# Kernel tuning notes

Hardware: AMD Instinct MI355X
Metric: run time of the kernel (lower is better)

Reference implementation:

```python
import jax, jax.numpy as jnp
import numpy as np

EMBED_DIM = 768
NUM_HEADS = 12
HEAD_DIM = EMBED_DIM // NUM_HEADS
SCALE = HEAD_DIM ** -0.5
LN_EPS = 1e-5


def layer_norm(x, gamma, beta):
    mu = jnp.mean(x, axis=-1, keepdims=True)
    var = jnp.var(x, axis=-1, keepdims=True)
    return (x - mu) * jax.lax.rsqrt(var + LN_EPS) * gamma + beta


def setup_inputs() -> dict:
    key = jax.random.key(0)
    ks = jax.random.split(key, 10)
    B, N, M, C = 4, 4096, 256, EMBED_DIM
    inp = {
        "input_tokens": jax.random.normal(ks[0], (B, N, C), dtype=jnp.float32),
        "query_tokens": jax.random.normal(ks[1], (B, M, C), dtype=jnp.float32),
        "Wq": jax.random.normal(ks[2], (C, C), dtype=jnp.float32) * 0.02,
        "bq": jnp.zeros((C,), dtype=jnp.float32),
        "Wk": jax.random.normal(ks[3], (C, C), dtype=jnp.float32) * 0.02,
        "bk": jnp.zeros((C,), dtype=jnp.float32),
        "Wv": jax.random.normal(ks[4], (C, C), dtype=jnp.float32) * 0.02,
        "bv": jnp.zeros((C,), dtype=jnp.float32),
        "gq_ln": jnp.ones((C,), dtype=jnp.float32),
        "bq_ln": jnp.zeros((C,), dtype=jnp.float32),
        "gk_ln": jnp.ones((C,), dtype=jnp.float32),
        "bk_ln": jnp.zeros((C,), dtype=jnp.float32),
    }
    return inp


def reference(input_tokens, query_tokens, Wq, bq, Wk, bk, Wv, bv,
              gq_ln, bq_ln, gk_ln, bk_ln):
    B, N, C = input_tokens.shape
    _, M, _ = query_tokens.shape
    H, D = NUM_HEADS, HEAD_DIM

    # v: Linear only (no LayerNorm on the attn=None path)
    v = (input_tokens @ Wv.T + bv).reshape(B, N, H, D).transpose(0, 2, 1, 3)   # [B,H,N,D]
    # q, k: Linear -> LayerNorm over full embed_dim, then split heads
    q = layer_norm(query_tokens @ Wq.T + bq, gq_ln, bq_ln)
    q = q.reshape(B, M, H, D).transpose(0, 2, 1, 3) * SCALE                    # [B,H,M,D]
    k = layer_norm(input_tokens @ Wk.T + bk, gk_ln, bk_ln)
    k = k.reshape(B, N, H, D).transpose(0, 2, 1, 3)                            # [B,H,N,D]

    attn = jax.nn.softmax(jnp.einsum('bhmd,bhnd->bhmn', q, k), axis=-1)        # [B,H,M,N]
    out = jnp.einsum('bhmn,bhnd->bhmd', attn, v)                               # [B,H,M,D]
    out = out.transpose(0, 2, 1, 3).reshape(B, M, C)
    return (query_tokens + out, attn)
```

## Files before the change

### kernel.cpp

```cpp
#include <hip/hip_runtime.h>
#include <math.h>

#define BB 4
#define NN 4096
#define MM 256
#define CC 768
#define HH 12
#define DD 64
#define SCALEF 0.125f
#define LN_EPSF 1e-5f

typedef __attribute__((ext_vector_type(4))) float f32x4;
typedef __attribute__((ext_vector_type(16))) float f32x16;
typedef __attribute__((ext_vector_type(8))) _Float16 f16x8;
typedef __attribute__((ext_vector_type(4))) _Float16 f16x4;

__device__ __forceinline__ void gldh(const _Float16* g, _Float16* l) {
    __builtin_amdgcn_global_load_lds(
        (const __attribute__((address_space(1))) void*)g,
        (__attribute__((address_space(3))) void*)l, 16, 0, 0);
}

__global__ __launch_bounds__(256) void conv_all(
    const float* __restrict__ x0, _Float16* __restrict__ y0, long long n0,
    const float* __restrict__ x1, _Float16* __restrict__ y1, long long n1,
    const float* __restrict__ x2, _Float16* __restrict__ y2, long long n2,
    const float* __restrict__ x3, _Float16* __restrict__ y3, long long n3,
    const float* __restrict__ x4, _Float16* __restrict__ y4, long long n4)
{
    long long i = ((long long)blockIdx.x * 256 + threadIdx.x) * 8;
    const long long total = n0 + n1 + n2 + n3 + n4;
    const long long stride = (long long)gridDim.x * 256 * 8;
    for (; i < total; i += stride) {
        const float* x; _Float16* y; long long off = i;
        if (off < n0) { x = x0; y = y0; }
        else if ((off -= n0) < n1) { x = x1; y = y1; }
        else if ((off -= n1) < n2) { x = x2; y = y2; }
        else if ((off -= n2) < n3) { x = x3; y = y3; }
        else { off -= n3; x = x4; y = y4; }
        float4 a = *(const float4*)(x + off);
        float4 b = *(const float4*)(x + off + 4);
        f16x8 o;
        o[0] = (_Float16)a.x; o[1] = (_Float16)a.y;
        o[2] = (_Float16)a.z; o[3] = (_Float16)a.w;
        o[4] = (_Float16)b.x; o[5] = (_Float16)b.y;
        o[6] = (_Float16)b.z; o[7] = (_Float16)b.w;
        *(f16x8*)(y + off) = o;
    }
}

__global__ __launch_bounds__(256) void proj_kv_f16(
    const _Float16* __restrict__ Xh,
    const _Float16* __restrict__ X2h,
    const _Float16* __restrict__ Wkh, const _Float16* __restrict__ Wqh,
    const _Float16* __restrict__ Wvh,
    const float* __restrict__ bk, const float* __restrict__ bq,
    const float* __restrict__ bv,
    _Float16* __restrict__ Klin, _Float16* __restrict__ Qlin,
    _Float16* __restrict__ Vth)
{
    __shared__ _Float16 As[2][4096];
    __shared__ _Float16 Bks[2][4096];
    __shared__ _Float16 Bvs[2][4096];

    const int bid = blockIdx.x;
    const _Float16* Ag; const _Float16* Bkg;
    const float* biask; _Float16* outk;
    bool hasV;
    int bm, bn;
    if (bid < 768) {
        bm = bid & 127; bn = bid >> 7;
        Ag = Xh; Bkg = Wkh; biask = bk; outk = Klin; hasV = true;
    } else {
        const int sid = bid - 768;
        bm = sid & 7; bn = sid >> 3;
        Ag = X2h; Bkg = Wqh; biask = bq; outk = Qlin; hasV = false;
    }
    const int row0 = bm * 128, col0 = bn * 128;

    const int tid = threadIdx.x;
    const int w = tid >> 6, lane = tid & 63;
    const int wr = w >> 1, wc = w & 1;
    const int fr = lane & 15, kg = lane >> 4;

    f32x4 acck[4][4], accv[4][4];
#pragma unroll
    for (int m = 0; m < 4; ++m)
#pragma unroll
        for (int n = 0; n < 4; ++n) {
            acck[m][n] = (f32x4){0.f, 0.f, 0.f, 0.f};
            accv[m][n] = (f32x4){0.f, 0.f, 0.f, 0.f};
        }

#define STAGE(sel, kt)                                                           \
    do {                                                                         \
        const int kk = (kt) << 5;                                                \
        _Pragma("unroll")                                                        \
        for (int i = 0; i < 2; ++i) {                                            \
            const int cbase = (i * 4 + w) * 64;                                  \
            const int c = cbase + lane;                                          \
            const int row = c >> 2, ks = (c & 3) << 3;                           \
            gldh(Ag  + (size_t)(row0 + row) * CC + kk + ks, &As[sel][cbase * 8]);\
            gldh(Bkg + (size_t)(col0 + row) * CC + kk + ks, &Bks[sel][cbase * 8]);\
            gldh(Wvh + (size_t)(col0 + row) * CC + kk + ks, &Bvs[sel][cbase * 8]);\
        }                                                                        \
    } while (0)

    STAGE(0, 0);
    int cur = 0;
    const int nk = CC >> 5;
    for (int kt = 0; kt < nk; ++kt) {
        __syncthreads();
        if (kt + 1 < nk) STAGE(cur ^ 1, kt + 1);
        const _Float16* lA = As[cur];
        const _Float16* lBk = Bks[cur];
        const _Float16* lBv = Bvs[cur];
        f16x8 a[4];
#pragma unroll
        for (int m = 0; m < 4; ++m)
            a[m] = *(const f16x8*)(lA + (wr * 64 + m * 16 + fr) * 32 + kg * 8);
#pragma unroll
        for (int n = 0; n < 4; ++n) {
            f16x8 bkf = *(const f16x8*)(lBk + (wc * 64 + n * 16 + fr) * 32 + kg * 8);
            __builtin_amdgcn_s_setprio(1);
#pragma unroll
            for (int m = 0; m < 4; ++m)
                acck[m][n] = __builtin_amdgcn_mfma_f32_16x16x32_f16(
                    a[m], bkf, acck[m][n], 0, 0, 0);
            __builtin_amdgcn_s_setprio(0);
            f16x8 bvf = *(const f16x8*)(lBv + (wc * 64 + n * 16 + fr) * 32 + kg * 8);
            __builtin_amdgcn_s_setprio(1);
#pragma unroll
            for (int m = 0; m < 4; ++m)
                accv[m][n] = __builtin_amdgcn_mfma_f32_16x16x32_f16(
                    a[m], bvf, accv[m][n], 0, 0, 0);
            __builtin_amdgcn_s_setprio(0);
        }
        cur ^= 1;
    }
#undef STAGE

    {
        float bvv[4];
#pragma unroll
        for (int n = 0; n < 4; ++n)
            bvv[n] = biask[col0 + wc * 64 + n * 16 + fr];
#pragma unroll
        for (int m = 0; m < 4; ++m)
#pragma unroll
            for (int n = 0; n < 4; ++n) {
                const int col = col0 + wc * 64 + n * 16 + fr;
#pragma unroll
                for (int r = 0; r < 4; ++r) {
                    const int row = row0 + wr * 64 + m * 16 + kg * 4 + r;
                    outk[(size_t)row * CC + col] = (_Float16)(acck[m][n][r] + bvv[n]);
                }
            }
    }
    if (hasV) {
        const int b = row0 >> 12;
        const int rb = row0 & 4095;
#pragma unroll
        for (int n = 0; n < 4; ++n) {
            const int cg = col0 + wc * 64 + n * 16 + fr;
            const int hh = cg >> 6, d = cg & 63;
            const float bb = bv[cg];
            _Float16* vrow = Vth + ((size_t)((b * HH + hh) * DD + d)) * NN + rb + wr * 64;
#pragma unroll
            for (int m = 0; m < 4; ++m) {
                f16x4 v4;
#pragma unroll
                for (int r = 0; r < 4; ++r)
                    v4[r] = (_Float16)(accv[m][n][r] + bb);
                *(f16x4*)(vrow + m * 16 + kg * 4) = v4;
            }
        }
    }
}

__global__ __launch_bounds__(256) void ln_rows_f16(
    const _Float16* __restrict__ Y, _Float16* __restrict__ outh,
    const float* __restrict__ g, const float* __restrict__ be, const float scale)
{
    const int row = blockIdx.x;
    const _Float16* y = Y + (size_t)row * CC;
    const int tid = threadIdx.x;
    float x0 = (float)y[tid], x1 = (float)y[tid + 256], x2 = (float)y[tid + 512];
    float s = x0 + x1 + x2;
    float q = x0 * x0 + x1 * x1 + x2 * x2;
#pragma unroll
    for (int o = 32; o >= 1; o >>= 1) {
        s += __shfl_xor(s, o, 64);
        q += __shfl_xor(q, o, 64);
    }
    __shared__ float sh_s[4], sh_q[4];
    const int w = tid >> 6;
    if ((tid & 63) == 0) { sh_s[w] = s; sh_q[w] = q; }
    __syncthreads();
    s = sh_s[0] + sh_s[1] + sh_s[2] + sh_s[3];
    q = sh_q[0] + sh_q[1] + sh_q[2] + sh_q[3];
    const float mu  = s * (1.f / 768.f);
    const float var = q * (1.f / 768.f) - mu * mu;
    const float inv = rsqrtf(var + LN_EPSF);
    _Float16* o = outh + (size_t)row * CC;
    o[tid]       = (_Float16)(((x0 - mu) * inv * g[tid]       + be[tid])       * scale);
    o[tid + 256] = (_Float16)(((x1 - mu) * inv * g[tid + 256] + be[tid + 256]) * scale);
    o[tid + 512] = (_Float16)(((x2 - mu) * inv * g[tid + 512] + be[tid + 512]) * scale);
}

__global__ __launch_bounds__(256, 4) void attn_stats(
    const _Float16* __restrict__ Qh,
    const _Float16* __restrict__ Kh,
    float* __restrict__ stats)
{
    __shared__ __align__(16) unsigned char smem[37888];
    _Float16* Kl = (_Float16*)smem;
    _Float16* Ql = (_Float16*)(smem + 32768);
    float (*red)[32][2] = (float(*)[32][2])(smem + 36864);

    const int tid = threadIdx.x;
    const int w = tid >> 6, lane = tid & 63;
    const int l5 = lane >> 5, lm = lane & 31;
    const int bid = blockIdx.x;
    const int mt = bid / 192;
    const int rem = bid % 192;
    const int bh = rem >> 2, ns = rem & 3;
    const int h = bh % HH, b = bh / HH;
    const int qr0 = mt * 32;
    const int nb = ns * 1024;

#define STAGEK(sel, c0)                                                         \
    _Pragma("unroll")                                                           \
    for (int i = 0; i < 4; ++i) {                                               \
        const int L = i * 256 + tid;                                            \
        const int n = L >> 3, pos = L & 7;                                      \
        gldh(Kh + (size_t)(b * NN + (c0) + n) * CC + h * DD + ((pos ^ (n & 7)) << 3), \
             &Kl[(sel) * 8192 + (i * 256 + w * 64) * 8]);                       \
    }

    {
        const int n = tid >> 3, pos = tid & 7;
        gldh(Qh + (size_t)(b * MM + qr0 + n) * CC + h * DD + ((pos ^ (n & 7)) << 3),
             &Ql[(w * 64) * 8]);
    }
    STAGEK(0, nb);
    __syncthreads();
    f16x8 qf[4];
#pragma unroll
    for (int ks = 0; ks < 4; ++ks)
        qf[ks] = *(const f16x8*)&Ql[lm * 64 + (((ks * 2 + l5) ^ (lm & 7)) << 3)];

    const int nl = w * 32 + lm;

    float mrun = -1e30f, srun = 0.f;
    int cur = 0;
    for (int c = 0; c < 8; ++c) {
        if (c) __syncthreads();
        if (c + 1 < 8) STAGEK(cur ^ 1, nb + (c + 1) * 128);
        const _Float16* Kb = Kl + cur * 8192;
        f32x16 s;
#pragma unroll
        for (int r = 0; r < 16; ++r) s[r] = 0.f;
        __builtin_amdgcn_s_setprio(1);
#pragma unroll
        for (int ks = 0; ks < 4; ++ks) {
            f16x8 kf = *(const f16x8*)&Kb[nl * 64 + (((ks * 2 + l5) ^ (nl & 7)) << 3)];
            s = __builtin_amdgcn_mfma_f32_32x32x16_f16(kf, qf[ks], s, 0, 0, 0);
        }
        __builtin_amdgcn_s_setprio(0);
        float cmax = s[0];
#pragma unroll
        for (int r = 1; r < 16; ++r) cmax = fmaxf(cmax, s[r]);
        cmax = fmaxf(cmax, __shfl_xor(cmax, 32, 64));
        const float nm = fmaxf(mrun, cmax);
        float cs = 0.f;
#pragma unroll
        for (int r = 0; r < 16; ++r) cs += __expf(s[r] - nm);
        cs += __shfl_xor(cs, 32, 64);
        srun = srun * __expf(mrun - nm) + cs;
        mrun = nm;
        cur ^= 1;
    }
    if (lane < 32) { red[w][lane][0] = mrun; red[w][lane][1] = srun; }
    __syncthreads();
    if (w == 0 && lane < 32) {
        float M = -1e30f;
#pragma unroll
        for (int ww = 0; ww < 4; ++ww) M = fmaxf(M, red[ww][lane][0]);
        float S = 0.f;
#pragma unroll
        for (int ww = 0; ww < 4; ++ww) S += red[ww][lane][1] * __expf(red[ww][lane][0] - M);
        float* sp = stats + ((size_t)((bh * 8 + mt) * 32 + lane)) * 8 + ns * 2;
        sp[0] = M; sp[1] = S;
    }
#undef STAGEK
}

__global__ __launch_bounds__(256, 2) void attn_main(
    const _Float16* __restrict__ Qh, const _Float16* __restrict__ Kh,
    const _Float16* __restrict__ Vt,
    const float* __restrict__ stats, const float* __restrict__ qtok,
    float* __restrict__ attn, float* __restrict__ out0)
{
    __shared__ __align__(16) unsigned char smem[77824];
    _Float16* Kl = (_Float16*)smem;
    _Float16* Vl = (_Float16*)(smem + 32768);
    _Float16* Ql = (_Float16*)(smem + 65536);
    _Float16* Pl = (_Float16*)(smem + 69632);
    float* rbuf = (float*)smem;

    const int tid = threadIdx.x;
    const int w = tid >> 6, lane = tid & 63;
    const int l5 = lane >> 5, lm = lane & 31;
    const int bh = blockIdx.x % 48;
    const int mt = blockIdx.x / 48;
    const int h = bh % HH, b = bh / HH;
    const int qr0 = mt * 32;

#define STAGEK(sel, c0)                                                         \
    _Pragma("unroll")                                                           \
    for (int i = 0; i < 4; ++i) {                                               \
        const int L = i * 256 + tid;                                            \
        const int n = L >> 3, pos = L & 7;                                      \
        gldh(Kh + (size_t)(b * NN + (c0) + n) * CC + h * DD + ((pos ^ (n & 7)) << 3), \
             &Kl[(sel) * 8192 + (i * 256 + w * 64) * 8]);                       \
    }
#define STAGEV(sel, c0)                                                         \
    _Pragma("unroll")                                                           \
    for (int i = 0; i < 4; ++i) {                                               \
        const int L = i * 256 + tid;                                            \
        const int d = L >> 4, pos = L & 15;                                     \
        const int blk = (pos & 8) | ((pos & 7) ^ (d & 7));                      \
        gldh(Vt + (size_t)(bh * DD + d) * NN + (c0) + blk * 8,                  \
             &Vl[(sel) * 8192 + (i * 256 + w * 64) * 8]);                       \
    }

    float M, invS;
    {
        const float* sp = stats + ((size_t)((bh * 8 + mt) * 32 + lm)) * 8;
        M = -1e30f;
#pragma unroll
        for (int n2 = 0; n2 < 4; ++n2) M = fmaxf(M, sp[n2 * 2]);
        float S = 0.f;
#pragma unroll
        for (int n2 = 0; n2 < 4; ++n2) S += sp[n2 * 2 + 1] * __expf(sp[n2 * 2] - M);
        invS = 1.f / S;
    }

    {
        const int n = tid >> 3, pos = tid & 7;
        gldh(Qh + (size_t)(b * MM + qr0 + n) * CC + h * DD + ((pos ^ (n & 7)) << 3),
             &Ql[(w * 64) * 8]);
    }
    STAGEK(0, 0); STAGEV(0, 0);
    __syncthreads();
    f16x8 qf[4];
#pragma unroll
    for (int ks = 0; ks < 4; ++ks)
        qf[ks] = *(const f16x8*)&Ql[lm * 64 + (((ks * 2 + l5) ^ (lm & 7)) << 3)];

    const int nl = w * 32 + lm;

    f32x16 oacc[2];
#pragma unroll
    for (int dt = 0; dt < 2; ++dt)
#pragma unroll
        for (int r = 0; r < 16; ++r) oacc[dt][r] = 0.f;

    int cur = 0;
    for (int c = 0; c < 32; ++c) {
        if (c) {
            asm volatile("s_waitcnt vmcnt(4)" ::: "memory");
            __builtin_amdgcn_s_barrier();
            __builtin_amdgcn_sched_barrier(0);
        }
        if (c + 1 < 32) { STAGEK(cur ^ 1, (c + 1) * 128); STAGEV(cur ^ 1, (c + 1) * 128); }
        __builtin_amdgcn_sched_barrier(0);
        const _Float16* Kb = Kl + cur * 8192;
        const _Float16* Vb = Vl + cur * 8192;
        f32x16 s;
#pragma unroll
        for (int r = 0; r < 16; ++r) s[r] = 0.f;
        __builtin_amdgcn_s_setprio(1);
#pragma unroll
        for (int ks = 0; ks < 4; ++ks) {
            f16x8 kf = *(const f16x8*)&Kb[nl * 64 + (((ks * 2 + l5) ^ (nl & 7)) << 3)];
            s = __builtin_amdgcn_mfma_f32_32x32x16_f16(kf, qf[ks], s, 0, 0, 0);
        }
        __builtin_amdgcn_s_setprio(0);
#pragma unroll
        for (int q = 0; q < 4; ++q) {
            f16x4 ph;
#pragma unroll
            for (int r = 0; r < 4; ++r)
                ph[r] = (_Float16)(__expf(s[q * 4 + r] - M) * invS);
            const int blk16 = w * 4 + q;
            const int pos = (blk16 & 8) | ((blk16 & 7) ^ (lm & 7));
            *(f16x4*)&Pl[lm * 128 + pos * 8 + l5 * 4] = ph;
        }
        __builtin_amdgcn_s_setprio(1);
#pragma unroll
        for (int ks = 0; ks < 2; ++ks) {
            const int blk16 = w * 4 + ks * 2 + l5;
            const int posP = (blk16 & 8) | ((blk16 & 7) ^ (lm & 7));
            f16x8 pf = *(const f16x8*)&Pl[lm * 128 + posP * 8];
#pragma unroll
            for (int dt = 0; dt < 2; ++dt) {
                const int d = dt * 32 + lm;
                const int posV = (blk16 & 8) | ((blk16 & 7) ^ (d & 7));
                f16x8 vf = *(const f16x8*)&Vb[d * 128 + posV * 8];
                oacc[dt] = __builtin_amdgcn_mfma_f32_32x32x16_f16(pf, vf, oacc[dt], 0, 0, 0);
            }
        }
        __builtin_amdgcn_s_setprio(0);
#pragma unroll
        for (int p = 0; p < 4; ++p) {
            const int pr = p >> 1, nh = p & 1;
            const int row = pr * 16 + (lane >> 2);
            const int k = lane & 3;
            const int nn = nh * 16 + k * 4;
            const int j = w * 4 + (nn >> 3);
            const int swz = (j & 8) | ((j & 7) ^ (row & 7));
            f16x4 pv4 = *(const f16x4*)&Pl[row * 128 + swz * 8 + (nn & 7)];
            f32x4 o4;
            o4[0] = (float)pv4[0]; o4[1] = (float)pv4[1];
            o4[2] = (float)pv4[2]; o4[3] = (float)pv4[3];
            __builtin_nontemporal_store(o4,
                (f32x4*)(attn + ((size_t)(bh * MM + qr0 + row)) * NN
                         + c * 128 + w * 32 + nn));
        }
        cur ^= 1;
    }

    __syncthreads();
#pragma unroll
    for (int dt = 0; dt < 2; ++dt)
#pragma unroll
        for (int r = 0; r < 16; ++r) {
            const int mrow = (r & 3) + 8 * (r >> 2) + 4 * l5;
            rbuf[w * 2048 + mrow * 64 + dt * 32 + lm] = oacc[dt][r];
        }
    __syncthreads();
    {
        const int m = tid >> 3, d0 = (tid & 7) * 8;
        const size_t obase = (size_t)(b * MM + qr0 + m) * CC + h * DD + d0;
        f32x4 v0, v1;
#pragma unroll
        for (int j = 0; j < 4; ++j) {
            const int idx = m * 64 + d0 + j;
            v0[j] = rbuf[idx] + rbuf[2048 + idx] + rbuf[4096 + idx] + rbuf[6144 + idx];
        }
#pragma unroll
        for (int j = 0; j < 4; ++j) {
            const int idx = m * 64 + d0 + 4 + j;
            v1[j] = rbuf[idx] + rbuf[2048 + idx] + rbuf[4096 + idx] + rbuf[6144 + idx];
        }
        float4 q0 = *(const float4*)(qtok + obase);
        float4 q1 = *(const float4*)(qtok + obase + 4);
        v0[0] += q0.x; v0[1] += q0.y; v0[2] += q0.z; v0[3] += q0.w;
        v1[0] += q1.x; v1[1] += q1.y; v1[2] += q1.z; v1[3] += q1.w;
        *(f32x4*)(out0 + obase) = v0;
        *(f32x4*)(out0 + obase + 4) = v1;
    }
#undef STAGEK
#undef STAGEV
}

extern "C" void kernel_launch(void* const* d_in, const int* in_sizes, int n_in,
                              void* d_out, int out_size, void* d_ws, size_t ws_size,
                              hipStream_t stream) {
    (void)in_sizes; (void)n_in; (void)out_size; (void)ws_size;
    const float* input_tokens = (const float*)d_in[0];
    const float* query_tokens = (const float*)d_in[1];
    const float* Wq   = (const float*)d_in[2];
    const float* bq   = (const float*)d_in[3];
    const float* Wk   = (const float*)d_in[4];
    const float* bk   = (const float*)d_in[5];
    const float* Wv   = (const float*)d_in[6];
    const float* bv   = (const float*)d_in[7];
    const float* gq   = (const float*)d_in[8];
    const float* bqln = (const float*)d_in[9];
    const float* gk   = (const float*)d_in[10];
    const float* bkln = (const float*)d_in[11];

    float* out0 = (float*)d_out;
    float* attn = out0 + (size_t)BB * MM * CC;

    _Float16* hptr = (_Float16*)d_ws;
    _Float16* Klin = hptr;
    _Float16* Qlin = Klin + (size_t)BB * NN * CC;
    _Float16* Xh   = Qlin + (size_t)BB * MM * CC;
    _Float16* X2h  = Xh   + (size_t)BB * NN * CC;
    _Float16* Wkh  = X2h  + (size_t)BB * MM * CC;
    _Float16* Wqh  = Wkh  + (size_t)CC * CC;
    _Float16* Wvh  = Wqh  + (size_t)CC * CC;
    _Float16* Kh   = Wvh  + (size_t)CC * CC;
    _Float16* Qh   = Kh   + (size_t)BB * NN * CC;
    _Float16* Vt   = Qh   + (size_t)BB * MM * CC;
    float* stats   = (float*)(Vt + (size_t)BB * HH * DD * NN);

    conv_all<<<2048, 256, 0, stream>>>(
        input_tokens, Xh, (long long)BB * NN * CC,
        query_tokens, X2h, (long long)BB * MM * CC,
        Wk, Wkh, (long long)CC * CC,
        Wq, Wqh, (long long)CC * CC,
        Wv, Wvh, (long long)CC * CC);

    proj_kv_f16<<<816, 256, 0, stream>>>(Xh, X2h, Wkh, Wqh, Wvh,
                                         bk, bq, bv, Klin, Qlin, Vt);

    ln_rows_f16<<<BB * NN, 256, 0, stream>>>(Klin, Kh, gk, bkln, 1.0f);
    ln_rows_f16<<<BB * MM, 256, 0, stream>>>(Qlin, Qh, gq, bqln, SCALEF);

    attn_stats<<<1536, 256, 0, stream>>>(Qh, Kh, stats);
    attn_main<<<384, 256, 0, stream>>>(Qh, Kh, Vt, stats, query_tokens, attn, out0);
}
```

Measured before the change: 187.6 us.

## Triple-buffer projection GEMM with explicit vmcnt waits and merge LayerNorm launches

The K/V/Q projection GEMM moves from double to triple LDS buffering, prefetching two k-tiles ahead. It replaces __syncthreads with an explicit s_waitcnt vmcnt plus s_barrier, so loads for later stages can stay in flight while the current tile is computed. The two LayerNorm launches (K rows and Q rows) are merged into one grid to save a kernel launch and its tail. The larger LDS footprint (72KB per block) may reduce how many blocks fit per CU, and the hand-set vmcnt count depends on how many loads each stage issues.

```diff
diff --git a/kernel.cpp b/kernel.cpp
--- a/kernel.cpp
+++ b/kernel.cpp
@@ -59,9 +59,9 @@
     _Float16* __restrict__ Klin, _Float16* __restrict__ Qlin,
     _Float16* __restrict__ Vth)
 {
-    __shared__ _Float16 As[2][4096];
-    __shared__ _Float16 Bks[2][4096];
-    __shared__ _Float16 Bvs[2][4096];
+    __shared__ _Float16 As[3][4096];
+    __shared__ _Float16 Bks[3][4096];
+    __shared__ _Float16 Bvs[3][4096];
 
     const int bid = blockIdx.x;
     const _Float16* Ag; const _Float16* Bkg;
@@ -107,11 +107,15 @@
     } while (0)
 
     STAGE(0, 0);
-    int cur = 0;
+    STAGE(1, 1);
     const int nk = CC >> 5;
     for (int kt = 0; kt < nk; ++kt) {
-        __syncthreads();
-        if (kt + 1 < nk) STAGE(cur ^ 1, kt + 1);
+        if (kt + 1 < nk) asm volatile("s_waitcnt vmcnt(6)" ::: "memory");
+        else             asm volatile("s_waitcnt vmcnt(0)" ::: "memory");
+        __builtin_amdgcn_s_barrier();
+        __builtin_amdgcn_sched_barrier(0);
+        if (kt + 2 < nk) STAGE((kt + 2) % 3, kt + 2);
+        const int cur = kt % 3;
         const _Float16* lA = As[cur];
         const _Float16* lBk = Bks[cur];
         const _Float16* lBv = Bvs[cur];
@@ -136,7 +140,6 @@
                     a[m], bvf, accv[m][n], 0, 0, 0);
             __builtin_amdgcn_s_setprio(0);
         }
-        cur ^= 1;
     }
 #undef STAGE
 
@@ -179,19 +182,30 @@
 }
 
 __global__ __launch_bounds__(256) void ln_rows_f16(
-    const _Float16* __restrict__ Y, _Float16* __restrict__ outh,
-    const float* __restrict__ g, const float* __restrict__ be, const float scale)
+    const _Float16* __restrict__ Klin, const _Float16* __restrict__ Qlin,
+    _Float16* __restrict__ Kh, _Float16* __restrict__ Qh,
+    const float* __restrict__ gk, const float* __restrict__ bkln,
+    const float* __restrict__ gq, const float* __restrict__ bqln)
 {
-    const int row = blockIdx.x;
-    const _Float16* y = Y + (size_t)row * CC;
+    int row = blockIdx.x;
+    const _Float16* y; _Float16* o;
+    const float* g; const float* be; float scale;
+    if (row < BB * NN) {
+        y = Klin + (size_t)row * CC; o = Kh + (size_t)row * CC;
+        g = gk; be = bkln; scale = 1.0f;
+    } else {
+        row -= BB * NN;
+        y = Qlin + (size_t)row * CC; o = Qh + (size_t)row * CC;
+        g = gq; be = bqln; scale = SCALEF;
+    }
     const int tid = threadIdx.x;
     float x0 = (float)y[tid], x1 = (float)y[tid + 256], x2 = (float)y[tid + 512];
     float s = x0 + x1 + x2;
     float q = x0 * x0 + x1 * x1 + x2 * x2;
 #pragma unroll
-    for (int o = 32; o >= 1; o >>= 1) {
-        s += __shfl_xor(s, o, 64);
-        q += __shfl_xor(q, o, 64);
+    for (int o2 = 32; o2 >= 1; o2 >>= 1) {
+        s += __shfl_xor(s, o2, 64);
+        q += __shfl_xor(q, o2, 64);
     }
     __shared__ float sh_s[4], sh_q[4];
     const int w = tid >> 6;
@@ -202,7 +216,6 @@
     const float mu  = s * (1.f / 768.f);
     const float var = q * (1.f / 768.f) - mu * mu;
     const float inv = rsqrtf(var + LN_EPSF);
-    _Float16* o = outh + (size_t)row * CC;
     o[tid]       = (_Float16)(((x0 - mu) * inv * g[tid]       + be[tid])       * scale);
     o[tid + 256] = (_Float16)(((x1 - mu) * inv * g[tid + 256] + be[tid + 256]) * scale);
     o[tid + 512] = (_Float16)(((x2 - mu) * inv * g[tid + 512] + be[tid + 512]) * scale);
@@ -509,8 +522,8 @@
     proj_kv_f16<<<816, 256, 0, stream>>>(Xh, X2h, Wkh, Wqh, Wvh,
                                          bk, bq, bv, Klin, Qlin, Vt);
 
-    ln_rows_f16<<<BB * NN, 256, 0, stream>>>(Klin, Kh, gk, bkln, 1.0f);
-    ln_rows_f16<<<BB * MM, 256, 0, stream>>>(Qlin, Qh, gq, bqln, SCALEF);
+    ln_rows_f16<<<BB * NN + BB * MM, 256, 0, stream>>>(Klin, Qlin, Kh, Qh,
+                                                       gk, bkln, gq, bqln);
 
     attn_stats<<<1536, 256, 0, stream>>>(Qh, Kh, stats);
     attn_main<<<384, 256, 0, stream>>>(Qh, Kh, Vt, stats, query_tokens, attn, out0);
```

Result: no change. 186.5 us (-0.6%).
